# Optimization experiments

Measured on AMD Instinct MI355X. Metric: run time of the kernel, lower is better.

Reference implementation:

```python
import jax, jax.numpy as jnp
import numpy as np

N_NODES = 100000
N_EDGES = 1600000
IN, HID, OUT = 128, 64, 64


def setup_inputs() -> dict:
    key = jax.random.key(0)
    ks = jax.random.split(key, 7)
    features = jax.random.normal(ks[0], (N_NODES, IN), dtype=jnp.float32)
    src = jax.random.randint(ks[1], (N_EDGES,), 0, N_NODES, dtype=jnp.int64)
    dst = jax.random.randint(ks[2], (N_EDGES,), 0, N_NODES, dtype=jnp.int64)
    # glorot-uniform-like init for GraphConv weights
    lim1 = np.sqrt(6.0 / (IN + HID)).astype(np.float32)
    lim2 = np.sqrt(6.0 / (HID + OUT)).astype(np.float32)
    W1 = jax.random.uniform(ks[3], (IN, HID), jnp.float32, -lim1, lim1)
    b1 = jnp.zeros((HID,), jnp.float32)
    W2 = jax.random.uniform(ks[4], (HID, OUT), jnp.float32, -lim2, lim2)
    b2 = jnp.zeros((OUT,), jnp.float32)
    return {"features": features, "src": src, "dst": dst,
            "W1": W1, "b1": b1, "W2": W2, "b2": b2}


def _graph_conv(h, W, b, src, dst, out_norm, in_norm, relu, n_nodes):
    # DGL GraphConv, norm='both':
    #   h_src *= outdeg^{-1/2}; aggregate sum over edges; h_dst *= indeg^{-1/2}
    #   W applied before aggregation if in_feats > out_feats (fewer bytes moved)
    h = h * out_norm[:, None]
    if h.shape[1] > W.shape[1]:
        h = h @ W
        agg = jax.ops.segment_sum(h[src], dst, num_segments=n_nodes)
    else:
        agg = jax.ops.segment_sum(h[src], dst, num_segments=n_nodes)
        agg = agg @ W
    out = agg * in_norm[:, None] + b
    return jax.nn.relu(out) if relu else out


def reference(features, src, dst, W1, b1, W2, b2):
    n_nodes = features.shape[0]
    ones = jnp.ones(src.shape[0], features.dtype)
    out_deg = jnp.maximum(jax.ops.segment_sum(ones, src, num_segments=n_nodes), 1.0)
    in_deg = jnp.maximum(jax.ops.segment_sum(ones, dst, num_segments=n_nodes), 1.0)
    out_norm = jax.lax.rsqrt(out_deg)
    in_norm = jax.lax.rsqrt(in_deg)
    h = _graph_conv(features, W1, b1, src, dst, out_norm, in_norm, True, n_nodes)
    # Dropout(0.5) between layers: identity in eval mode
    h = _graph_conv(h, W2, b2, src, dst, out_norm, in_norm, False, n_nodes)
    return h
```

## Files before the change

### kernel.cpp

```cpp
#include <hip/hip_runtime.h>
#include <hip/hip_fp16.h>

#define NCH 64
#define INF 128
#define PAD 64
#define HQD 128
#define HQS 64
#define NPH 2
#define CHUNK_H 50000
#define NPF 4
#define CHUNK_F 25000

using ivec4 = __attribute__((ext_vector_type(4))) int;
using hvec8 = __attribute__((ext_vector_type(8))) _Float16;
using fvec8 = __attribute__((ext_vector_type(8))) float;
using half8 = __attribute__((ext_vector_type(8))) _Float16;
using f32x4 = __attribute__((ext_vector_type(4))) float;

__global__ __launch_bounds__(512) void k_hist2(
    const int* __restrict__ src, const int* __restrict__ dst,
    unsigned char* __restrict__ shist, unsigned char* __restrict__ dhist,
    int nE, int nN) {
    __shared__ unsigned cnt[CHUNK_H / 4];
    const int dstBlocks = NPH * HQD;
    const bool isDst = (int)blockIdx.x < dstBlocks;
    const int bid = isDst ? blockIdx.x : blockIdx.x - dstBlocks;
    const int* __restrict__ arr = isDst ? dst : src;
    unsigned char* __restrict__ hist = isDst ? dhist : shist;
    const int HQX = isDst ? HQD : HQS;
    const int p = bid & (NPH - 1);
    const int q = bid >> 1;
    const int lo = p * CHUNK_H;
    for (int i = threadIdx.x; i < CHUNK_H / 4; i += 512) cnt[i] = 0;
    __syncthreads();
    const int nE4 = nE >> 2;
    const int b0 = (int)(((long)q * nE4) / HQX);
    const int b1 = (int)(((long)(q + 1) * nE4) / HQX);
    for (int i = b0 + threadIdx.x; i < b1; i += 512) {
        ivec4 v4 = __builtin_nontemporal_load(((const ivec4*)arr) + i);
#pragma unroll
        for (int j = 0; j < 4; ++j) {
            int x = v4[j] - lo;
            if ((unsigned)x < (unsigned)CHUNK_H)
                atomicAdd(&cnt[x >> 2], 1u << ((x & 3) * 8));
        }
    }
    if (q == 0 && threadIdx.x < (nE & 3)) {
        int x = arr[(nE4 << 2) + threadIdx.x] - lo;
        if ((unsigned)x < (unsigned)CHUNK_H)
            atomicAdd(&cnt[x >> 2], 1u << ((x & 3) * 8));
    }
    __syncthreads();
    unsigned* hp = (unsigned*)(hist + (long)q * nN + lo);
    int lim = nN - lo;
    if (lim > CHUNK_H) lim = CHUNK_H;
    lim >>= 2;
    for (int i = threadIdx.x; i < lim; i += 512) hp[i] = cnt[i];
}

__global__ void k_scan2(const unsigned char* __restrict__ shist,
                        unsigned char* __restrict__ dhist,
                        float* __restrict__ onorm, int* __restrict__ indeg, int nN) {
    int n = blockIdx.x * blockDim.x + threadIdx.x;
    if (n >= nN) return;
    int s = 0;
#pragma unroll 4
    for (int q = 0; q < HQS; ++q) s += shist[(long)q * nN + n];
    onorm[n] = rsqrtf(fmaxf((float)s, 1.0f));
    int run = 0;
    for (int q = 0; q < HQD; ++q) {
        long idx = (long)q * nN + n;
        int v = dhist[idx];
        dhist[idx] = (unsigned char)run;
        run += v;
    }
    indeg[n] = run;
}

__global__ __launch_bounds__(512) void k_fill(
    const int* __restrict__ src, const int* __restrict__ dst,
    const unsigned char* __restrict__ qoff, int* __restrict__ ell, int nE, int nN) {
    __shared__ unsigned cnt[CHUNK_F / 4];
    const int p = blockIdx.x & (NPF - 1);
    const int q = blockIdx.x >> 2;
    const int lo = p * CHUNK_F;
    const unsigned* qw = (const unsigned*)(qoff + (long)q * nN + lo);
    for (int i = threadIdx.x; i < CHUNK_F / 4; i += 512) cnt[i] = qw[i];
    __syncthreads();
    const int nE4 = nE >> 2;
    const int b0 = (int)(((long)q * nE4) / HQD);
    const int b1 = (int)(((long)(q + 1) * nE4) / HQD);
    for (int i = b0 + threadIdx.x; i < b1; i += 512) {
        ivec4 s4 = __builtin_nontemporal_load(((const ivec4*)src) + i);
        ivec4 d4 = __builtin_nontemporal_load(((const ivec4*)dst) + i);
#pragma unroll
        for (int j = 0; j < 4; ++j) {
            int d = d4[j] - lo;
            if ((unsigned)d < (unsigned)CHUNK_F) {
                int sh = (d & 3) * 8;
                unsigned old = atomicAdd(&cnt[d >> 2], 1u << sh);
                int pos = (old >> sh) & 0xff;
                if (pos < PAD) ell[(long)(lo + d) * PAD + pos] = s4[j];
            }
        }
    }
    if (q == 0 && threadIdx.x < (nE & 3)) {
        int e = (nE4 << 2) + threadIdx.x;
        int d = dst[e] - lo;
        if ((unsigned)d < (unsigned)CHUNK_F) {
            int sh = (d & 3) * 8;
            unsigned old = atomicAdd(&cnt[d >> 2], 1u << sh);
            int pos = (old >> sh) & 0xff;
            if (pos < PAD) ell[(long)(lo + d) * PAD + pos] = src[e];
        }
    }
}

__global__ __launch_bounds__(256) void k_gemm1m(
    const float* __restrict__ feat, const float* __restrict__ W1,
    const float* __restrict__ onorm, __half* __restrict__ h1, int nN)
{
    const int lane = threadIdx.x & 63;
    const int row_in = lane & 15;
    const int kgrp = lane >> 4;
    half8 bf[4][4];
#pragma unroll
    for (int ks = 0; ks < 4; ++ks)
#pragma unroll
        for (int g = 0; g < 4; ++g) {
            int col = g * 16 + row_in;
#pragma unroll
            for (int j = 0; j < 8; ++j)
                bf[ks][g][j] = (_Float16)W1[(ks * 32 + kgrp * 8 + j) * NCH + col];
        }
    const int nTiles = (nN + 15) >> 4;
    int tile = blockIdx.x * 4 + (threadIdx.x >> 6);
    const int stride = gridDim.x * 4;
    for (; tile < nTiles; tile += stride) {
        const long r0 = (long)tile * 16;
        const long ra = r0 + row_in;
        half8 af[4];
        if (ra < nN) {
#pragma unroll
            for (int ks = 0; ks < 4; ++ks) {
                const float* fp = feat + ra * INF + ks * 32 + kgrp * 8;
                float4 x = *(const float4*)fp;
                float4 y = *(const float4*)(fp + 4);
                af[ks][0] = (_Float16)x.x; af[ks][1] = (_Float16)x.y;
                af[ks][2] = (_Float16)x.z; af[ks][3] = (_Float16)x.w;
                af[ks][4] = (_Float16)y.x; af[ks][5] = (_Float16)y.y;
                af[ks][6] = (_Float16)y.z; af[ks][7] = (_Float16)y.w;
            }
        } else {
#pragma unroll
            for (int ks = 0; ks < 4; ++ks)
#pragma unroll
                for (int j = 0; j < 8; ++j) af[ks][j] = (_Float16)0.0f;
        }
        f32x4 acc[4] = {{0,0,0,0},{0,0,0,0},{0,0,0,0},{0,0,0,0}};
#pragma unroll
        for (int ks = 0; ks < 4; ++ks)
#pragma unroll
            for (int g = 0; g < 4; ++g)
                acc[g] = __builtin_amdgcn_mfma_f32_16x16x32_f16(af[ks], bf[ks][g], acc[g], 0, 0, 0);
#pragma unroll
        for (int j = 0; j < 4; ++j) {
            long r = r0 + kgrp * 4 + j;
            if (r < nN) {
                float on = onorm[r];
#pragma unroll
                for (int g = 0; g < 4; ++g)
                    h1[r * NCH + g * 16 + row_in] = __float2half(acc[g][j] * on);
            }
        }
    }
}

__global__ __launch_bounds__(256) void k_agg1(
    const __half* __restrict__ h1s, const int* __restrict__ indeg,
    const int* __restrict__ ell, const float* __restrict__ onorm,
    const float* __restrict__ b1, __half* __restrict__ h2, int nN)
{
    const int c = threadIdx.x & 7;
    int node = (blockIdx.x << 5) + (threadIdx.x >> 3);
    if (node >= nN) return;
    int n0 = indeg[node];
    int n = (n0 > PAD) ? PAD : n0;
    const int* cols = ell + (long)node * PAD;
    fvec8 acc = {0, 0, 0, 0, 0, 0, 0, 0};
    int i = 0;
    for (; i + 4 <= n; i += 4) {
        int s0 = cols[i], s1 = cols[i + 1], s2 = cols[i + 2], s3 = cols[i + 3];
        hvec8 v0 = ((const hvec8*)h1s)[(long)s0 * 8 + c];
        hvec8 v1 = ((const hvec8*)h1s)[(long)s1 * 8 + c];
        hvec8 v2 = ((const hvec8*)h1s)[(long)s2 * 8 + c];
        hvec8 v3 = ((const hvec8*)h1s)[(long)s3 * 8 + c];
#pragma unroll
        for (int j = 0; j < 8; ++j)
            acc[j] += (float)v0[j] + (float)v1[j] + (float)v2[j] + (float)v3[j];
    }
    for (; i < n; ++i) {
        hvec8 v = ((const hvec8*)h1s)[(long)cols[i] * 8 + c];
#pragma unroll
        for (int j = 0; j < 8; ++j) acc[j] += (float)v[j];
    }
    float inn = rsqrtf(fmaxf((float)n0, 1.0f));
    float onn = onorm[node];
    float4 ba = ((const float4*)b1)[2 * c];
    float4 bb = ((const float4*)b1)[2 * c + 1];
    float bv[8] = {ba.x, ba.y, ba.z, ba.w, bb.x, bb.y, bb.z, bb.w};
    hvec8 st;
#pragma unroll
    for (int j = 0; j < 8; ++j)
        st[j] = (_Float16)(fmaxf(acc[j] * inn + bv[j], 0.0f) * onn);
    ((hvec8*)h2)[(long)node * 8 + c] = st;
}

__global__ __launch_bounds__(256) void k_agg2(
    const __half* __restrict__ h2, const int* __restrict__ indeg,
    const int* __restrict__ ell, __half* __restrict__ agg, int nN)
{
    const int c = threadIdx.x & 7;
    int node = (blockIdx.x << 5) + (threadIdx.x >> 3);
    if (node >= nN) return;
    int n0 = indeg[node];
    int n = (n0 > PAD) ? PAD : n0;
    const int* cols = ell + (long)node * PAD;
    fvec8 acc = {0, 0, 0, 0, 0, 0, 0, 0};
    int i = 0;
    for (; i + 4 <= n; i += 4) {
        int s0 = cols[i], s1 = cols[i + 1], s2 = cols[i + 2], s3 = cols[i + 3];
        hvec8 v0 = ((const hvec8*)h2)[(long)s0 * 8 + c];
        hvec8 v1 = ((const hvec8*)h2)[(long)s1 * 8 + c];
        hvec8 v2 = ((const hvec8*)h2)[(long)s2 * 8 + c];
        hvec8 v3 = ((const hvec8*)h2)[(long)s3 * 8 + c];
#pragma unroll
        for (int j = 0; j < 8; ++j)
            acc[j] += (float)v0[j] + (float)v1[j] + (float)v2[j] + (float)v3[j];
    }
    for (; i < n; ++i) {
        hvec8 v = ((const hvec8*)h2)[(long)cols[i] * 8 + c];
#pragma unroll
        for (int j = 0; j < 8; ++j) acc[j] += (float)v[j];
    }
    hvec8 st;
#pragma unroll
    for (int j = 0; j < 8; ++j) st[j] = (_Float16)acc[j];
    ((hvec8*)agg)[(long)node * 8 + c] = st;
}

__global__ __launch_bounds__(256) void k_gemm2m(
    const __half* __restrict__ agg, const float* __restrict__ W2,
    const int* __restrict__ indeg, const float* __restrict__ b2,
    float* __restrict__ out, int nN)
{
    const int lane = threadIdx.x & 63;
    const int row_in = lane & 15;
    const int kgrp = lane >> 4;
    half8 bf[2][4];
#pragma unroll
    for (int ks = 0; ks < 2; ++ks)
#pragma unroll
        for (int g = 0; g < 4; ++g) {
            int col = g * 16 + row_in;
#pragma unroll
            for (int j = 0; j < 8; ++j)
                bf[ks][g][j] = (_Float16)W2[(ks * 32 + kgrp * 8 + j) * NCH + col];
        }
    float bcol[4];
#pragma unroll
    for (int g = 0; g < 4; ++g) bcol[g] = b2[g * 16 + row_in];
    const int nTiles = (nN + 15) >> 4;
    int tile = blockIdx.x * 4 + (threadIdx.x >> 6);
    const int stride = gridDim.x * 4;
    for (; tile < nTiles; tile += stride) {
        const long r0 = (long)tile * 16;
        const long ra = r0 + row_in;
        half8 af[2];
        if (ra < nN) {
#pragma unroll
            for (int ks = 0; ks < 2; ++ks)
                af[ks] = ((const half8*)agg)[ra * 8 + ks * 4 + kgrp];
        } else {
#pragma unroll
            for (int ks = 0; ks < 2; ++ks)
#pragma unroll
                for (int j = 0; j < 8; ++j) af[ks][j] = (_Float16)0.0f;
        }
        f32x4 acc[4] = {{0,0,0,0},{0,0,0,0},{0,0,0,0},{0,0,0,0}};
#pragma unroll
        for (int ks = 0; ks < 2; ++ks)
#pragma unroll
            for (int g = 0; g < 4; ++g)
                acc[g] = __builtin_amdgcn_mfma_f32_16x16x32_f16(af[ks], bf[ks][g], acc[g], 0, 0, 0);
#pragma unroll
        for (int j = 0; j < 4; ++j) {
            long r = r0 + kgrp * 4 + j;
            if (r < nN) {
                float inn = rsqrtf(fmaxf((float)indeg[r], 1.0f));
#pragma unroll
                for (int g = 0; g < 4; ++g)
                    out[r * NCH + g * 16 + row_in] = acc[g][j] * inn + bcol[g];
            }
        }
    }
}

extern "C" void kernel_launch(void* const* d_in, const int* in_sizes, int n_in,
                              void* d_out, int out_size, void* d_ws, size_t ws_size,
                              hipStream_t stream) {
    const float* feat = (const float*)d_in[0];
    const int* src    = (const int*)d_in[1];
    const int* dst    = (const int*)d_in[2];
    const float* W1   = (const float*)d_in[3];
    const float* b1   = (const float*)d_in[4];
    const float* W2   = (const float*)d_in[5];
    const float* b2   = (const float*)d_in[6];
    float* out        = (float*)d_out;

    const int nN = in_sizes[0] / INF;
    const int nE = in_sizes[1];

    char* p = (char*)d_ws;
    float* onorm  = (float*)p;   p += (size_t)nN * 4;
    int* indeg    = (int*)p;     p += (size_t)nN * 4;
    char* unionp  = p;           p += (size_t)nN * NCH * 2 * 2;
    int* ell      = (int*)p;     p += (size_t)nN * PAD * 4;
    unsigned char* shist = (unsigned char*)unionp;
    unsigned char* dhist = (unsigned char*)unionp + (size_t)HQS * nN;
    __half* h2    = (__half*)unionp;
    __half* agg2  = (__half*)(unionp + (size_t)nN * NCH * 2);
    __half* h1    = (__half*)d_out;

    k_hist2<<<NPH * HQD + NPH * HQS, 512, 0, stream>>>(src, dst, shist, dhist, nE, nN);

    k_scan2<<<(nN + 255) / 256, 256, 0, stream>>>(shist, dhist, onorm, indeg, nN);

    k_gemm1m<<<1024, 256, 0, stream>>>(feat, W1, onorm, h1, nN);

    k_fill<<<NPF * HQD, 512, 0, stream>>>(src, dst, dhist, ell, nE, nN);

    k_agg1<<<(nN + 31) / 32, 256, 0, stream>>>(h1, indeg, ell, onorm, b1, h2, nN);

    k_agg2<<<(nN + 31) / 32, 256, 0, stream>>>(h2, indeg, ell, agg2, nN);

    k_gemm2m<<<512, 256, 0, stream>>>(agg2, W2, indeg, b2, out, nN);
}
```

Baseline: 168.6 us.

## Bucket nodes by in-degree so aggregation waves process similar-degree nodes

Adds a two-pass counting sort that builds a permutation of nodes grouped by in-degree (capped at 64 buckets), and makes both aggregation kernels process nodes in that order. The intent is to reduce divergence within a wavefront, since the 8-thread groups for different nodes in a wave have different loop trip counts. It costs a memset, two small sort kernels, and an extra indirection in the aggregation kernels. It also gives up the locality of writing outputs in node order, since stores now follow the permuted order.

```diff
diff --git a/kernel.cpp b/kernel.cpp
--- a/kernel.cpp
+++ b/kernel.cpp
@@ -10,6 +10,8 @@
 #define CHUNK_H 50000
 #define NPF 4
 #define CHUNK_F 25000
+#define NB 64
+#define SORT_NPB 1024
 
 using ivec4 = __attribute__((ext_vector_type(4))) int;
 using hvec8 = __attribute__((ext_vector_type(8))) _Float16;
@@ -77,6 +79,49 @@
     indeg[n] = run;
 }
 
+__global__ __launch_bounds__(256) void k_sort1(
+    const int* __restrict__ indeg, int* __restrict__ gcnt,
+    int* __restrict__ bbase, int nN) {
+    __shared__ int lcnt[NB];
+    if (threadIdx.x < NB) lcnt[threadIdx.x] = 0;
+    __syncthreads();
+    int base = blockIdx.x * SORT_NPB;
+#pragma unroll
+    for (int j = 0; j < 4; ++j) {
+        int n = base + j * 256 + threadIdx.x;
+        if (n < nN) {
+            int b = indeg[n]; if (b > NB - 1) b = NB - 1;
+            atomicAdd(&lcnt[b], 1);
+        }
+    }
+    __syncthreads();
+    if (threadIdx.x < NB)
+        bbase[blockIdx.x * NB + threadIdx.x] = atomicAdd(&gcnt[threadIdx.x], lcnt[threadIdx.x]);
+}
+
+__global__ __launch_bounds__(256) void k_sort3(
+    const int* __restrict__ indeg, const int* __restrict__ gcnt,
+    const int* __restrict__ bbase, int* __restrict__ perm, int nN) {
+    __shared__ int gs[NB];
+    __shared__ int lcnt[NB];
+    if (threadIdx.x == 0) {
+        int run = 0;
+        for (int b = 0; b < NB; ++b) { gs[b] = run; run += gcnt[b]; }
+    }
+    if (threadIdx.x < NB) lcnt[threadIdx.x] = 0;
+    __syncthreads();
+    int base = blockIdx.x * SORT_NPB;
+#pragma unroll
+    for (int j = 0; j < 4; ++j) {
+        int n = base + j * 256 + threadIdx.x;
+        if (n < nN) {
+            int b = indeg[n]; if (b > NB - 1) b = NB - 1;
+            int rank = atomicAdd(&lcnt[b], 1);
+            perm[gs[b] + bbase[blockIdx.x * NB + b] + rank] = n;
+        }
+    }
+}
+
 __global__ __launch_bounds__(512) void k_fill(
     const int* __restrict__ src, const int* __restrict__ dst,
     const unsigned char* __restrict__ qoff, int* __restrict__ ell, int nE, int nN) {
@@ -179,11 +224,13 @@
 __global__ __launch_bounds__(256) void k_agg1(
     const __half* __restrict__ h1s, const int* __restrict__ indeg,
     const int* __restrict__ ell, const float* __restrict__ onorm,
-    const float* __restrict__ b1, __half* __restrict__ h2, int nN)
+    const float* __restrict__ b1, __half* __restrict__ h2,
+    const int* __restrict__ perm, int nN)
 {
     const int c = threadIdx.x & 7;
-    int node = (blockIdx.x << 5) + (threadIdx.x >> 3);
-    if (node >= nN) return;
+    int slot = (blockIdx.x << 5) + (threadIdx.x >> 3);
+    if (slot >= nN) return;
+    int node = perm[slot];
     int n0 = indeg[node];
     int n = (n0 > PAD) ? PAD : n0;
     const int* cols = ell + (long)node * PAD;
@@ -218,11 +265,13 @@
 
 __global__ __launch_bounds__(256) void k_agg2(
     const __half* __restrict__ h2, const int* __restrict__ indeg,
-    const int* __restrict__ ell, __half* __restrict__ agg, int nN)
+    const int* __restrict__ ell, __half* __restrict__ agg,
+    const int* __restrict__ perm, int nN)
 {
     const int c = threadIdx.x & 7;
-    int node = (blockIdx.x << 5) + (threadIdx.x >> 3);
-    if (node >= nN) return;
+    int slot = (blockIdx.x << 5) + (threadIdx.x >> 3);
+    if (slot >= nN) return;
+    int node = perm[slot];
     int n0 = indeg[node];
     int n = (n0 > PAD) ? PAD : n0;
     const int* cols = ell + (long)node * PAD;
@@ -320,29 +369,38 @@
 
     const int nN = in_sizes[0] / INF;
     const int nE = in_sizes[1];
+    const int nSortBlk = (nN + SORT_NPB - 1) / SORT_NPB;
 
     char* p = (char*)d_ws;
     float* onorm  = (float*)p;   p += (size_t)nN * 4;
     int* indeg    = (int*)p;     p += (size_t)nN * 4;
     char* unionp  = p;           p += (size_t)nN * NCH * 2 * 2;
     int* ell      = (int*)p;     p += (size_t)nN * PAD * 4;
+    int* perm     = (int*)p;     p += (size_t)nN * 4;
+    int* gcnt     = (int*)p;     p += (size_t)NB * 4;
+    int* bbase    = (int*)p;     p += (size_t)nSortBlk * NB * 4;
     unsigned char* shist = (unsigned char*)unionp;
     unsigned char* dhist = (unsigned char*)unionp + (size_t)HQS * nN;
     __half* h2    = (__half*)unionp;
     __half* agg2  = (__half*)(unionp + (size_t)nN * NCH * 2);
     __half* h1    = (__half*)d_out;
 
+    (void)hipMemsetAsync(gcnt, 0, (size_t)NB * 4, stream);
+
     k_hist2<<<NPH * HQD + NPH * HQS, 512, 0, stream>>>(src, dst, shist, dhist, nE, nN);
 
     k_scan2<<<(nN + 255) / 256, 256, 0, stream>>>(shist, dhist, onorm, indeg, nN);
 
+    k_sort1<<<nSortBlk, 256, 0, stream>>>(indeg, gcnt, bbase, nN);
+    k_sort3<<<nSortBlk, 256, 0, stream>>>(indeg, gcnt, bbase, perm, nN);
+
     k_gemm1m<<<1024, 256, 0, stream>>>(feat, W1, onorm, h1, nN);
 
     k_fill<<<NPF * HQD, 512, 0, stream>>>(src, dst, dhist, ell, nE, nN);
 
-    k_agg1<<<(nN + 31) / 32, 256, 0, stream>>>(h1, indeg, ell, onorm, b1, h2, nN);
-
-    k_agg2<<<(nN + 31) / 32, 256, 0, stream>>>(h2, indeg, ell, agg2, nN);
+    k_agg1<<<(nN + 31) / 32, 256, 0, stream>>>(h1, indeg, ell, onorm, b1, h2, perm, nN);
+
+    k_agg2<<<(nN + 31) / 32, 256, 0, stream>>>(h2, indeg, ell, agg2, perm, nN);
 
     k_gemm2m<<<512, 256, 0, stream>>>(agg2, W2, indeg, b2, out, nN);
 }
```

Result: slower. 181.3 us (+7.5%).
